# Optimization experiments

Hardware: AMD Instinct MI355X
Metric: run time of the kernel (lower is better)

## Reference

```python
import jax, jax.numpy as jnp
import numpy as np

UNITS = 32
ATT_WIDTH = 64


def setup_inputs() -> dict:
    key = jax.random.key(0)
    ks = jax.random.split(key, 4)
    B, T, F = 4, 1024, 256
    x = jax.random.normal(ks[0], (B, T, F), dtype=jnp.float32)
    Wt = jax.random.normal(ks[1], (F, UNITS), dtype=jnp.float32) * (1.0 / np.sqrt(F))
    Wx = jax.random.normal(ks[2], (F, UNITS), dtype=jnp.float32) * (1.0 / np.sqrt(F))
    bh = jnp.zeros((UNITS,), dtype=jnp.float32)
    Wa = jax.random.normal(ks[3], (UNITS, 1), dtype=jnp.float32) * (1.0 / np.sqrt(UNITS))
    ba = jnp.zeros((1,), dtype=jnp.float32)
    return {"x": x, "Wt": Wt, "Wx": Wx, "bh": bh, "Wa": Wa, "ba": ba}


def reference(x, Wt, Wx, bh, Wa, ba):
    # Additive (Bahdanau-style) self-attention emission:
    # h[b,t,s,u] = tanh(x[b,t] @ Wt + x[b,s] @ Wx + bh)
    q = jnp.einsum('btf,fu->btu', x, Wt)[:, :, None, :]   # [B,T,1,U]
    k = jnp.einsum('bsf,fu->bsu', x, Wx)[:, None, :, :]   # [B,1,T,U]
    h = jnp.tanh(q + k + bh)                               # [B,T,T,U]
    e = jnp.einsum('btsu,uo->bts', h, Wa) + ba[0]          # [B,T,T]

    # Local attention window (symmetric, width=ATT_WIDTH)
    T = x.shape[1]
    idx = jnp.arange(T)
    lower = idx - ATT_WIDTH // 2                           # [T]
    band = (lower[:, None] <= idx[None, :]) & (idx[None, :] < lower[:, None] + ATT_WIDTH)
    e = e - 10000.0 * (1.0 - band.astype(e.dtype))

    a = jax.nn.softmax(e, axis=-1)                         # [B,T,T]
    v = jnp.einsum('bts,bsf->btf', a, x)                   # [B,T,F]
    return v
```

## Files before the change

kernel.cpp:

```cpp
#include <hip/hip_runtime.h>
#include <math.h>

#define BB 4
#define TT 1024
#define FF 256
#define UU 32
#define HALF_W 32
#define WMAX 64

__global__ __launch_bounds__(64) void qk_kernel(
    const float* __restrict__ x, const float* __restrict__ Wt,
    const float* __restrict__ Wx, const float* __restrict__ bh,
    float* __restrict__ qbuf, float* __restrict__ kbuf) {
    int row = blockIdx.x;
    int tid = threadIdx.x;
    __shared__ float xs[FF];
    ((float4*)xs)[tid] = ((const float4*)(x + (size_t)row * FF))[tid];
    __syncthreads();
    int u = tid & 31;
    const float* W = (tid < 32) ? Wt : Wx;
    float acc = 0.f;
#pragma unroll 8
    for (int f = 0; f < FF; ++f)
        acc += xs[f] * W[f * UU + u];
    if (tid < 32) qbuf[row * UU + u] = acc + bh[u];
    else          kbuf[row * UU + u] = acc;
}

__global__ __launch_bounds__(256) void attn_kernel(
    const float* __restrict__ x, const float* __restrict__ qbuf,
    const float* __restrict__ kbuf, const float* __restrict__ Wa,
    const float* __restrict__ ba, float* __restrict__ out) {
    int row = blockIdx.x;
    int t = row & (TT - 1);
    int b = row >> 10;
    int tid = threadIdx.x;
    int s0 = max(0, t - HALF_W);
    int s1 = min(TT, t + HALF_W);
    int W_ = s1 - s0;

    __shared__ float q_sh[UU];
    __shared__ float wa_sh[UU];
    __shared__ float e_sh[WMAX];
    __shared__ float a_sh[WMAX];

    if (tid < UU) {
        q_sh[tid]  = qbuf[row * UU + tid];
        wa_sh[tid] = Wa[tid];
    }
    __syncthreads();

    int sl = tid >> 2;
    int j  = tid & 3;
    float partial = 0.f;
    if (sl < W_) {
        const float* krow = kbuf + (size_t)(b * TT + s0 + sl) * UU + j * 8;
#pragma unroll
        for (int uu = 0; uu < 8; ++uu) {
            int u = j * 8 + uu;
            partial += tanhf(q_sh[u] + krow[uu]) * wa_sh[u];
        }
    }
    partial += __shfl_xor(partial, 1);
    partial += __shfl_xor(partial, 2);
    if (j == 0) e_sh[sl] = (sl < W_) ? partial + ba[0] : -1e30f;
    __syncthreads();

    if (tid < 64) {
        float e = e_sh[tid];
        float m = e;
#pragma unroll
        for (int off = 1; off < 64; off <<= 1) m = fmaxf(m, __shfl_xor(m, off));
        float p = __expf(e - m);
        float sum = p;
#pragma unroll
        for (int off = 1; off < 64; off <<= 1) sum += __shfl_xor(sum, off);
        a_sh[tid] = p / sum;
    }
    __syncthreads();

    float acc = 0.f;
    const float* xb = x + (size_t)(b * TT + s0) * FF + tid;
    for (int k2 = 0; k2 < W_; ++k2)
        acc += a_sh[k2] * xb[(size_t)k2 * FF];
    out[(size_t)row * FF + tid] = acc;
}

__global__ __launch_bounds__(256) void fused_kernel(
    const float* __restrict__ x, const float* __restrict__ Wt,
    const float* __restrict__ Wx, const float* __restrict__ bh,
    const float* __restrict__ Wa, const float* __restrict__ ba,
    float* __restrict__ out) {
    int row = blockIdx.x;
    int t = row & (TT - 1);
    int b = row >> 10;
    int tid = threadIdx.x;
    int s0 = max(0, t - HALF_W);
    int s1 = min(TT, t + HALF_W);
    int W_ = s1 - s0;

    __shared__ float ks[WMAX * UU];
    __shared__ float q_sh[UU];
    __shared__ float wa_sh[UU];
    __shared__ float e_sh[WMAX];
    __shared__ float a_sh[WMAX];

    if (tid < UU) {
        const float* xr = x + (size_t)row * FF;
        float acc = 0.f;
        for (int f = 0; f < FF; ++f) acc += xr[f] * Wt[f * UU + tid];
        q_sh[tid]  = acc + bh[tid];
        wa_sh[tid] = Wa[tid];
    }
    for (int p = tid; p < W_ * UU; p += 256) {
        int sl = p >> 5, u = p & 31;
        const float* xr = x + (size_t)(b * TT + s0 + sl) * FF;
        float acc = 0.f;
        for (int f = 0; f < FF; ++f) acc += xr[f] * Wx[f * UU + u];
        ks[p] = acc;
    }
    __syncthreads();

    int sl = tid >> 2;
    int j  = tid & 3;
    float partial = 0.f;
    if (sl < W_) {
#pragma unroll
        for (int uu = 0; uu < 8; ++uu) {
            int u = j * 8 + uu;
            partial += tanhf(q_sh[u] + ks[sl * UU + u]) * wa_sh[u];
        }
    }
    partial += __shfl_xor(partial, 1);
    partial += __shfl_xor(partial, 2);
    if (j == 0) e_sh[sl] = (sl < W_) ? partial + ba[0] : -1e30f;
    __syncthreads();

    if (tid < 64) {
        float e = e_sh[tid];
        float m = e;
#pragma unroll
        for (int off = 1; off < 64; off <<= 1) m = fmaxf(m, __shfl_xor(m, off));
        float p = __expf(e - m);
        float sum = p;
#pragma unroll
        for (int off = 1; off < 64; off <<= 1) sum += __shfl_xor(sum, off);
        a_sh[tid] = p / sum;
    }
    __syncthreads();

    float acc = 0.f;
    const float* xb = x + (size_t)(b * TT + s0) * FF + tid;
    for (int k2 = 0; k2 < W_; ++k2)
        acc += a_sh[k2] * xb[(size_t)k2 * FF];
    out[(size_t)row * FF + tid] = acc;
}

extern "C" void kernel_launch(void* const* d_in, const int* in_sizes, int n_in,
                              void* d_out, int out_size, void* d_ws, size_t ws_size,
                              hipStream_t stream) {
    const float* x  = (const float*)d_in[0];
    const float* Wt = (const float*)d_in[1];
    const float* Wx = (const float*)d_in[2];
    const float* bh = (const float*)d_in[3];
    const float* Wa = (const float*)d_in[4];
    const float* ba = (const float*)d_in[5];
    float* out = (float*)d_out;

    const size_t need = (size_t)2 * BB * TT * UU * sizeof(float);
    if (ws_size >= need) {
        float* qbuf = (float*)d_ws;
        float* kbuf = qbuf + (size_t)BB * TT * UU;
        qk_kernel<<<BB * TT, 64, 0, stream>>>(x, Wt, Wx, bh, qbuf, kbuf);
        attn_kernel<<<BB * TT, 256, 0, stream>>>(x, qbuf, kbuf, Wa, ba, out);
    } else {
        fused_kernel<<<BB * TT, 256, 0, stream>>>(x, Wt, Wx, bh, Wa, ba, out);
    }
}
```

Baseline: 102.6 us.

## Batch four rows per qk block, use fast tanh, vectorize k loads

```diff
diff --git a/kernel.cpp b/kernel.cpp
--- a/kernel.cpp
+++ b/kernel.cpp
@@ -8,23 +8,36 @@
 #define HALF_W 32
 #define WMAX 64
 
-__global__ __launch_bounds__(64) void qk_kernel(
+__device__ __forceinline__ float fast_tanh(float x) {
+    float e = __expf(2.0f * x);
+    return 1.0f - 2.0f / (e + 1.0f);
+}
+
+__global__ __launch_bounds__(256) void qk_kernel(
     const float* __restrict__ x, const float* __restrict__ Wt,
     const float* __restrict__ Wx, const float* __restrict__ bh,
     float* __restrict__ qbuf, float* __restrict__ kbuf) {
-    int row = blockIdx.x;
+    int row0 = blockIdx.x * 4;
     int tid = threadIdx.x;
-    __shared__ float xs[FF];
-    ((float4*)xs)[tid] = ((const float4*)(x + (size_t)row * FF))[tid];
+    __shared__ float xs[4][FF];
+    {
+        int r = tid >> 6;
+        int c4 = tid & 63;
+        ((float4*)xs[r])[c4] = ((const float4*)(x + (size_t)(row0 + r) * FF))[c4];
+    }
     __syncthreads();
+    int r = tid >> 6;
+    int half = (tid >> 5) & 1;
     int u = tid & 31;
-    const float* W = (tid < 32) ? Wt : Wx;
+    const float* __restrict__ W = half ? Wx : Wt;
+    const float* __restrict__ xr = xs[r];
     float acc = 0.f;
 #pragma unroll 8
     for (int f = 0; f < FF; ++f)
-        acc += xs[f] * W[f * UU + u];
-    if (tid < 32) qbuf[row * UU + u] = acc + bh[u];
-    else          kbuf[row * UU + u] = acc;
+        acc = fmaf(xr[f], W[f * UU + u], acc);
+    int row = row0 + r;
+    if (half == 0) qbuf[row * UU + u] = acc + bh[u];
+    else           kbuf[row * UU + u] = acc;
 }
 
 __global__ __launch_bounds__(256) void attn_kernel(
@@ -54,12 +67,18 @@
     int j  = tid & 3;
     float partial = 0.f;
     if (sl < W_) {
-        const float* krow = kbuf + (size_t)(b * TT + s0 + sl) * UU + j * 8;
-#pragma unroll
-        for (int uu = 0; uu < 8; ++uu) {
-            int u = j * 8 + uu;
-            partial += tanhf(q_sh[u] + krow[uu]) * wa_sh[u];
-        }
+        const float4* krow = (const float4*)(kbuf + (size_t)(b * TT + s0 + sl) * UU + j * 8);
+        float4 k0 = krow[0];
+        float4 k1 = krow[1];
+        int u = j * 8;
+        partial  = fast_tanh(q_sh[u + 0] + k0.x) * wa_sh[u + 0];
+        partial += fast_tanh(q_sh[u + 1] + k0.y) * wa_sh[u + 1];
+        partial += fast_tanh(q_sh[u + 2] + k0.z) * wa_sh[u + 2];
+        partial += fast_tanh(q_sh[u + 3] + k0.w) * wa_sh[u + 3];
+        partial += fast_tanh(q_sh[u + 4] + k1.x) * wa_sh[u + 4];
+        partial += fast_tanh(q_sh[u + 5] + k1.y) * wa_sh[u + 5];
+        partial += fast_tanh(q_sh[u + 6] + k1.z) * wa_sh[u + 6];
+        partial += fast_tanh(q_sh[u + 7] + k1.w) * wa_sh[u + 7];
     }
     partial += __shfl_xor(partial, 1);
     partial += __shfl_xor(partial, 2);
@@ -81,8 +100,9 @@
 
     float acc = 0.f;
     const float* xb = x + (size_t)(b * TT + s0) * FF + tid;
+#pragma unroll 4
     for (int k2 = 0; k2 < W_; ++k2)
-        acc += a_sh[k2] * xb[(size_t)k2 * FF];
+        acc = fmaf(a_sh[k2], xb[(size_t)k2 * FF], acc);
     out[(size_t)row * FF + tid] = acc;
 }
 
@@ -108,7 +128,7 @@
     if (tid < UU) {
         const float* xr = x + (size_t)row * FF;
         float acc = 0.f;
-        for (int f = 0; f < FF; ++f) acc += xr[f] * Wt[f * UU + tid];
+        for (int f = 0; f < FF; ++f) acc = fmaf(xr[f], Wt[f * UU + tid], acc);
         q_sh[tid]  = acc + bh[tid];
         wa_sh[tid] = Wa[tid];
     }
@@ -116,7 +136,7 @@
         int sl = p >> 5, u = p & 31;
         const float* xr = x + (size_t)(b * TT + s0 + sl) * FF;
         float acc = 0.f;
-        for (int f = 0; f < FF; ++f) acc += xr[f] * Wx[f * UU + u];
+        for (int f = 0; f < FF; ++f) acc = fmaf(xr[f], Wx[f * UU + u], acc);
         ks[p] = acc;
     }
     __syncthreads();
@@ -128,7 +148,7 @@
 #pragma unroll
         for (int uu = 0; uu < 8; ++uu) {
             int u = j * 8 + uu;
-            partial += tanhf(q_sh[u] + ks[sl * UU + u]) * wa_sh[u];
+            partial += fast_tanh(q_sh[u] + ks[sl * UU + u]) * wa_sh[u];
         }
     }
     partial += __shfl_xor(partial, 1);
@@ -152,7 +172,7 @@
     float acc = 0.f;
     const float* xb = x + (size_t)(b * TT + s0) * FF + tid;
     for (int k2 = 0; k2 < W_; ++k2)
-        acc += a_sh[k2] * xb[(size_t)k2 * FF];
+        acc = fmaf(a_sh[k2], xb[(size_t)k2 * FF], acc);
     out[(size_t)row * FF + tid] = acc;
 }
 
@@ -171,7 +191,7 @@
     if (ws_size >= need) {
         float* qbuf = (float*)d_ws;
         float* kbuf = qbuf + (size_t)BB * TT * UU;
-        qk_kernel<<<BB * TT, 64, 0, stream>>>(x, Wt, Wx, bh, qbuf, kbuf);
+        qk_kernel<<<BB * TT / 4, 256, 0, stream>>>(x, Wt, Wx, bh, qbuf, kbuf);
         attn_kernel<<<BB * TT, 256, 0, stream>>>(x, qbuf, kbuf, Wa, ba, out);
     } else {
         fused_kernel<<<BB * TT, 256, 0, stream>>>(x, Wt, Wx, bh, Wa, ba, out);
```

Result: faster. 91.96 us (-10.4%).
